# Kernel tuning notes

Hardware: AMD Instinct MI355X
Metric: run time of the kernel (lower is better)

## Reference

```python
import jax, jax.numpy as jnp
import numpy as np

N_NODES = 50000


def gcn_conv(x, W, b, src, dst, n_nodes):
    """PyG GCNConv: h = D^-1/2 (A + I) D^-1/2 (x W) + b, with self-loops."""
    h = x @ W  # [N, out]
    loop = jnp.arange(n_nodes, dtype=src.dtype)
    s = jnp.concatenate([src, loop])  # [E+N]
    d = jnp.concatenate([dst, loop])
    # degree of destination nodes (self-loops guarantee deg >= 1)
    deg = jax.ops.segment_sum(jnp.ones_like(d, dtype=h.dtype), d, num_segments=n_nodes)
    dinv = jax.lax.rsqrt(deg)  # deg >= 1 so safe
    norm = dinv[s] * dinv[d]  # [E+N]
    msg = h[s] * norm[:, None]  # gather + scale (per-edge messages)
    out = jax.ops.segment_sum(msg, d, num_segments=n_nodes)  # scatter-add
    return out + b


def setup_inputs() -> dict:
    key = jax.random.key(0)
    ks = jax.random.split(key, 8)
    in_d, hid, out_d = 128, 128, 64
    x = jax.random.normal(ks[0], (N_NODES, in_d), dtype=jnp.float32)
    edge_index = jax.random.randint(ks[1], (2, 800000), 0, N_NODES, dtype=jnp.int64)
    def glorot(k, fan_in, fan_out):
        lim = float(np.sqrt(6.0 / (fan_in + fan_out)))
        return jax.random.uniform(k, (fan_in, fan_out), jnp.float32, -lim, lim)
    return {
        "x": x,
        "edge_index": edge_index,
        "W1": glorot(ks[2], in_d, hid),
        "b1": jnp.zeros((hid,), jnp.float32),
        "W2": glorot(ks[3], hid, hid),
        "b2": jnp.zeros((hid,), jnp.float32),
        "W3": glorot(ks[4], hid, out_d),
        "b3": jnp.zeros((out_d,), jnp.float32),
    }


def reference(x, edge_index, W1, b1, W2, b2, W3, b3):
    src, dst = edge_index[0], edge_index[1]
    n = x.shape[0]
    h = jax.nn.relu(gcn_conv(x, W1, b1, src, dst, n))
    h = jax.nn.relu(gcn_conv(h, W2, b2, src, dst, n))
    return gcn_conv(h, W3, b3, src, dst, n)
```

## Files before the change

kernel.cpp:

```cpp
#include <hip/hip_runtime.h>
#include <stdint.h>
#include <stddef.h>

#define EE 800000
#define CAP 64
#define FB_G 256

typedef __attribute__((ext_vector_type(8))) short bf16x8;
typedef __attribute__((ext_vector_type(4))) float f32x4;

__device__ __forceinline__ float bflo(uint32_t p) { return __uint_as_float(p << 16); }
__device__ __forceinline__ float bfhi(uint32_t p) { return __uint_as_float(p & 0xffff0000u); }
__device__ __forceinline__ unsigned short f2bf(float v) {
  uint32_t b = __float_as_uint(v);
  b += 0x7fffu + ((b >> 16) & 1u);
  return (unsigned short)(b >> 16);
}

__device__ __forceinline__ void wt_work(int idx, const float* W1, const float* W2,
                                        const float* W3, unsigned short* Wt1,
                                        unsigned short* Wt2, unsigned short* Wt3) {
  if (idx < 16384) {
    int k = idx >> 7, n = idx & 127;
    Wt1[n * 128 + k] = f2bf(W1[idx]);
  } else if (idx < 32768) {
    int l = idx - 16384, k = l >> 7, n = l & 127;
    Wt2[n * 128 + k] = f2bf(W2[l]);
  } else if (idx < 40960) {
    int l = idx - 32768, k = l >> 6, n = l & 63;
    Wt3[n * 128 + k] = f2bf(W3[l]);
  }
}

__global__ void k15_fillslot(const int* ei, int* cnt, int* slots, int E, int N,
                             int* viol, const float* W1, const float* W2,
                             const float* W3, unsigned short* Wt1,
                             unsigned short* Wt2, unsigned short* Wt3) {
  if ((int)blockIdx.x >= 8 * FB_G) {
    wt_work(((int)blockIdx.x - 8 * FB_G) * 256 + threadIdx.x, W1, W2, W3, Wt1,
            Wt2, Wt3);
    return;
  }
  const int p = (int)blockIdx.x & 7;
  const int cb = (int)blockIdx.x >> 3;
  const int lo = (int)(((long long)N * p) >> 3);
  const int hi = (int)(((long long)N * (p + 1)) >> 3);
  const bool is64 =
      ((ei[1] | ei[3] | ei[5] | ei[7] | ei[9] | ei[11] | ei[13] | ei[15]) == 0);
  const uint2* e64 = (const uint2*)ei;
  const int step = FB_G * 256;

  int e = cb * 256 + (int)threadIdx.x;
  if (e >= E) return;
  int d = is64 ? (int)e64[(size_t)E + e].x : ei[(size_t)E + e];
  for (;;) {
    int e2 = e + step;
    int d2 = 0;
    if (e2 < E) d2 = is64 ? (int)e64[(size_t)E + e2].x : ei[(size_t)E + e2];
    if (p == 0 && (unsigned)d >= (unsigned)N) atomicOr(viol, 1);
    if (d >= lo && d < hi) {
      int s = is64 ? (int)e64[(size_t)e].x : ei[e];
      if ((unsigned)s >= (unsigned)N) {
        atomicOr(viol, 1);
      } else {
        int pos = atomicAdd(&cnt[d], 1);
        if (pos < CAP) slots[(size_t)d * CAP + pos] = s;
      }
    }
    if (e2 >= E) break;
    e = e2;
    d = d2;
  }
}

__global__ __launch_bounds__(256) void k12_wt(const float* W1, const float* W2,
                                              const float* W3, unsigned short* Wt1,
                                              unsigned short* Wt2, unsigned short* Wt3) {
  wt_work(blockIdx.x * 256 + threadIdx.x, W1, W2, W3, Wt1, Wt2, Wt3);
}

__global__ void k12_hist(const int* ei, int* cnt, int E, int N, int* viol) {
  bool is64 = ((ei[1] | ei[3] | ei[5] | ei[7] | ei[9] | ei[11] | ei[13] | ei[15]) == 0);
  if (blockIdx.x == 0 && threadIdx.x == 0) viol[1] = is64 ? 1 : 0;
  int e = blockIdx.x * 256 + threadIdx.x;
  if (e >= E) return;
  int s, d;
  if (is64) {
    const uint2* e64 = (const uint2*)ei;
    s = (int)e64[e].x;
    d = (int)e64[(size_t)E + e].x;
  } else {
    s = ei[e];
    d = ei[(size_t)E + e];
  }
  if ((unsigned)s >= (unsigned)N || (unsigned)d >= (unsigned)N) {
    atomicOr(viol, 1);
    return;
  }
  atomicAdd(&cnt[d], 1);
}

__global__ __launch_bounds__(256) void k12_scanA(const int* cnt, int* partial, int N) {
  __shared__ int sc[256];
  int t = threadIdx.x;
  int n = blockIdx.x * 256 + t;
  sc[t] = (n < N) ? cnt[n] : 0;
  __syncthreads();
  for (int s = 128; s > 0; s >>= 1) {
    if (t < s) sc[t] += sc[t + s];
    __syncthreads();
  }
  if (t == 0) partial[blockIdx.x] = sc[0];
}

__global__ __launch_bounds__(256) void k12_scanB(int* partial, int* off, int nsb,
                                                 int N, int E, int* viol) {
  __shared__ int sc[256];
  int t = threadIdx.x;
  int v = (t < nsb) ? partial[t] : 0;
  sc[t] = v;
  __syncthreads();
  for (int d = 1; d < 256; d <<= 1) {
    int w = (t >= d) ? sc[t - d] : 0;
    __syncthreads();
    sc[t] += w;
    __syncthreads();
  }
  if (t < nsb) partial[t] = sc[t] - v;
  if (t == 255) {
    off[N] = sc[255];
    if (sc[255] != E) atomicOr(viol, 4);
  }
}

__global__ __launch_bounds__(256) void k12_scanC(const int* cnt, const int* partial,
                                                 int* off, int* cur, float* dinv, int N) {
  __shared__ int sc[256];
  int t = threadIdx.x;
  int n = blockIdx.x * 256 + t;
  int v = (n < N) ? cnt[n] : 0;
  sc[t] = v;
  __syncthreads();
  for (int d = 1; d < 256; d <<= 1) {
    int w = (t >= d) ? sc[t - d] : 0;
    __syncthreads();
    sc[t] += w;
    __syncthreads();
  }
  if (n < N) {
    int o = partial[blockIdx.x] + sc[t] - v;
    off[n] = o;
    cur[n] = o;
    dinv[n] = rsqrtf((float)(v + 1));
  }
}

__global__ void k12_fillcsr(const int* ei, int* cur, int* adj, int E, int N,
                            const int* viol) {
  int is64 = viol[1];
  int e = blockIdx.x * 256 + threadIdx.x;
  if (e >= E) return;
  int s, d;
  if (is64) {
    const uint2* e64 = (const uint2*)ei;
    s = (int)e64[e].x;
    d = (int)e64[(size_t)E + e].x;
  } else {
    s = ei[e];
    d = ei[(size_t)E + e];
  }
  if ((unsigned)s >= (unsigned)N || (unsigned)d >= (unsigned)N) return;
  int pos = atomicAdd(&cur[d], 1);
  adj[pos] = s;
}

__global__ __launch_bounds__(256) void k12_gemmX(const float* __restrict__ X,
                                                 const unsigned short* __restrict__ Wt,
                                                 unsigned short* __restrict__ OUT,
                                                 int M) {
  const int tid = threadIdx.x;
  const int wid = tid >> 6, lane = tid & 63;
  const int quad = lane >> 4, r16 = lane & 15;
  const int m0 = blockIdx.x * 64 + wid * 16;
  const int mrow = m0 + r16;

  f32x4 acc[8];
#pragma unroll
  for (int ct = 0; ct < 8; ++ct) acc[ct] = {0.f, 0.f, 0.f, 0.f};

#pragma unroll
  for (int kk = 0; kk < 4; ++kk) {
    bf16x8 a = {0, 0, 0, 0, 0, 0, 0, 0};
    if (mrow < M) {
      const float* xp = X + (size_t)mrow * 128 + kk * 32 + quad * 8;
      float4 u0 = *(const float4*)xp;
      float4 u1 = *(const float4*)(xp + 4);
      a[0] = (short)f2bf(u0.x); a[1] = (short)f2bf(u0.y);
      a[2] = (short)f2bf(u0.z); a[3] = (short)f2bf(u0.w);
      a[4] = (short)f2bf(u1.x); a[5] = (short)f2bf(u1.y);
      a[6] = (short)f2bf(u1.z); a[7] = (short)f2bf(u1.w);
    }
#pragma unroll
    for (int ct = 0; ct < 8; ++ct) {
      bf16x8 b = *(const bf16x8*)(Wt + (size_t)(ct * 16 + r16) * 128 + kk * 32 + quad * 8);
      acc[ct] = __builtin_amdgcn_mfma_f32_16x16x32_bf16(a, b, acc[ct], 0, 0, 0);
    }
  }
#pragma unroll
  for (int ct = 0; ct < 8; ++ct) {
    int col = ct * 16 + r16;
#pragma unroll
    for (int r = 0; r < 4; ++r) {
      int row = m0 + quad * 4 + r;
      if (row < M) OUT[(size_t)row * 128 + col] = f2bf(acc[ct][r]);
    }
  }
}

template <int F>
__global__ __launch_bounds__(256) void k12_gemmB(const unsigned short* __restrict__ X,
                                                 const unsigned short* __restrict__ Wt,
                                                 unsigned short* __restrict__ OUT,
                                                 int M) {
  const int tid = threadIdx.x;
  const int wid = tid >> 6, lane = tid & 63;
  const int quad = lane >> 4, r16 = lane & 15;
  const int m0 = blockIdx.x * 64 + wid * 16;
  const int mrow = m0 + r16;
  constexpr int CT = F / 16;

  f32x4 acc[CT];
#pragma unroll
  for (int ct = 0; ct < CT; ++ct) acc[ct] = {0.f, 0.f, 0.f, 0.f};

#pragma unroll
  for (int kk = 0; kk < 4; ++kk) {
    bf16x8 a = {0, 0, 0, 0, 0, 0, 0, 0};
    if (mrow < M) a = *(const bf16x8*)(X + (size_t)mrow * 128 + kk * 32 + quad * 8);
#pragma unroll
    for (int ct = 0; ct < CT; ++ct) {
      bf16x8 b = *(const bf16x8*)(Wt + (size_t)(ct * 16 + r16) * 128 + kk * 32 + quad * 8);
      acc[ct] = __builtin_amdgcn_mfma_f32_16x16x32_bf16(a, b, acc[ct], 0, 0, 0);
    }
  }
#pragma unroll
  for (int ct = 0; ct < CT; ++ct) {
    int col = ct * 16 + r16;
#pragma unroll
    for (int r = 0; r < 4; ++r) {
      int row = m0 + quad * 4 + r;
      if (row < M) OUT[(size_t)row * F + col] = f2bf(acc[ct][r]);
    }
  }
}

template <int SLOT>
__global__ __launch_bounds__(256) void k15_agg128(
    const unsigned short* __restrict__ t, const int* __restrict__ cntoff,
    const int* __restrict__ adj, const float* __restrict__ dinv,
    const float* __restrict__ bias, unsigned short* __restrict__ out,
    int N, int* __restrict__ viol) {
  __shared__ uint2 sm[4][68];
  const int wid = (int)threadIdx.x >> 6;
  const int lane = (int)threadIdx.x & 63;
  const int g = lane >> 4, l16 = lane & 15;
  const int i = blockIdx.x * 4 + wid;
  if (i >= N) return;

  int j0, deg;
  float di;
  if (SLOT) {
    int c = cntoff[i];
    di = rsqrtf((float)(c + 1));
    if (c > CAP) {
      if (lane == 0) atomicOr(viol, 2);
      c = CAP;
    }
    deg = c;
    j0 = i * CAP;
  } else {
    j0 = cntoff[i];
    deg = cntoff[i + 1] - j0;
    di = dinv[i];
  }

  const int L = deg + 1;
  const uint4* rows = (const uint4*)t;
  float a0 = 0.f, a1 = 0.f, a2 = 0.f, a3 = 0.f;
  float a4 = 0.f, a5 = 0.f, a6 = 0.f, a7 = 0.f;

  for (int jb = 0; jb < L; jb += 64) {
    int v = jb + lane;
    uint2 ent;
    ent.x = 0u;
    ent.y = 0u;
    if (v == 0) {
      ent.x = (uint32_t)i;
      ent.y = __float_as_uint(di);
    } else if (v <= deg) {
      int s = adj[j0 + v - 1];
      float w = SLOT ? rsqrtf((float)(cntoff[s] + 1)) : dinv[s];
      ent.x = (uint32_t)s;
      ent.y = __float_as_uint(w);
    }
    sm[wid][lane] = ent;
    int nb2 = L - jb;
    if (nb2 > 64) nb2 = 64;
    int r4 = (nb2 + 3) >> 2;
    int b = 0;
    for (; b + 2 <= r4; b += 2) {
      uint2 s0 = sm[wid][b * 4 + g];
      uint2 s1 = sm[wid][b * 4 + 4 + g];
      uint4 p0 = rows[(size_t)s0.x * 16 + l16];
      uint4 p1 = rows[(size_t)s1.x * 16 + l16];
      float w0 = __uint_as_float(s0.y), w1 = __uint_as_float(s1.y);
      a0 = fmaf(w0, bflo(p0.x), a0); a1 = fmaf(w0, bfhi(p0.x), a1);
      a2 = fmaf(w0, bflo(p0.y), a2); a3 = fmaf(w0, bfhi(p0.y), a3);
      a4 = fmaf(w0, bflo(p0.z), a4); a5 = fmaf(w0, bfhi(p0.z), a5);
      a6 = fmaf(w0, bflo(p0.w), a6); a7 = fmaf(w0, bfhi(p0.w), a7);
      a0 = fmaf(w1, bflo(p1.x), a0); a1 = fmaf(w1, bfhi(p1.x), a1);
      a2 = fmaf(w1, bflo(p1.y), a2); a3 = fmaf(w1, bfhi(p1.y), a3);
      a4 = fmaf(w1, bflo(p1.z), a4); a5 = fmaf(w1, bfhi(p1.z), a5);
      a6 = fmaf(w1, bflo(p1.w), a6); a7 = fmaf(w1, bfhi(p1.w), a7);
    }
    if (b < r4) {
      uint2 s0 = sm[wid][b * 4 + g];
      uint4 p0 = rows[(size_t)s0.x * 16 + l16];
      float w0 = __uint_as_float(s0.y);
      a0 = fmaf(w0, bflo(p0.x), a0); a1 = fmaf(w0, bfhi(p0.x), a1);
      a2 = fmaf(w0, bflo(p0.y), a2); a3 = fmaf(w0, bfhi(p0.y), a3);
      a4 = fmaf(w0, bflo(p0.z), a4); a5 = fmaf(w0, bfhi(p0.z), a5);
      a6 = fmaf(w0, bflo(p0.w), a6); a7 = fmaf(w0, bfhi(p0.w), a7);
    }
  }
#pragma unroll
  for (int sx = 16; sx < 64; sx <<= 1) {
    a0 += __shfl_xor(a0, sx); a1 += __shfl_xor(a1, sx);
    a2 += __shfl_xor(a2, sx); a3 += __shfl_xor(a3, sx);
    a4 += __shfl_xor(a4, sx); a5 += __shfl_xor(a5, sx);
    a6 += __shfl_xor(a6, sx); a7 += __shfl_xor(a7, sx);
  }
  if (g == 0) {
    const float4* bf = (const float4*)bias;
    float4 b0 = bf[l16 * 2], b1 = bf[l16 * 2 + 1];
    a0 = fmaxf(fmaf(a0, di, b0.x), 0.f);
    a1 = fmaxf(fmaf(a1, di, b0.y), 0.f);
    a2 = fmaxf(fmaf(a2, di, b0.z), 0.f);
    a3 = fmaxf(fmaf(a3, di, b0.w), 0.f);
    a4 = fmaxf(fmaf(a4, di, b1.x), 0.f);
    a5 = fmaxf(fmaf(a5, di, b1.y), 0.f);
    a6 = fmaxf(fmaf(a6, di, b1.z), 0.f);
    a7 = fmaxf(fmaf(a7, di, b1.w), 0.f);
    uint4 pk;
    pk.x = (uint32_t)f2bf(a0) | ((uint32_t)f2bf(a1) << 16);
    pk.y = (uint32_t)f2bf(a2) | ((uint32_t)f2bf(a3) << 16);
    pk.z = (uint32_t)f2bf(a4) | ((uint32_t)f2bf(a5) << 16);
    pk.w = (uint32_t)f2bf(a6) | ((uint32_t)f2bf(a7) << 16);
    ((uint4*)out)[(size_t)i * 16 + l16] = pk;
  }
}

template <int SLOT>
__global__ __launch_bounds__(256) void k15_agg64(
    const unsigned short* __restrict__ t, const int* __restrict__ cntoff,
    const int* __restrict__ adj, const float* __restrict__ dinv,
    const float* __restrict__ bias, float* __restrict__ out,
    int N, int* __restrict__ viol) {
  __shared__ uint2 sm[4][68];
  const int wid = (int)threadIdx.x >> 6;
  const int lane = (int)threadIdx.x & 63;
  const int g = lane >> 4, l16 = lane & 15;
  const int i = blockIdx.x * 4 + wid;
  if (i >= N) return;

  int j0, deg;
  float di;
  if (SLOT) {
    int c = cntoff[i];
    di = rsqrtf((float)(c + 1));
    if (c > CAP) {
      if (lane == 0) atomicOr(viol, 2);
      c = CAP;
    }
    deg = c;
    j0 = i * CAP;
  } else {
    j0 = cntoff[i];
    deg = cntoff[i + 1] - j0;
    di = dinv[i];
  }

  const int L = deg + 1;
  const uint2* rows = (const uint2*)t;
  float a0 = 0.f, a1 = 0.f, a2 = 0.f, a3 = 0.f;

  for (int jb = 0; jb < L; jb += 64) {
    int v = jb + lane;
    uint2 ent;
    ent.x = 0u;
    ent.y = 0u;
    if (v == 0) {
      ent.x = (uint32_t)i;
      ent.y = __float_as_uint(di);
    } else if (v <= deg) {
      int s = adj[j0 + v - 1];
      float w = SLOT ? rsqrtf((float)(cntoff[s] + 1)) : dinv[s];
      ent.x = (uint32_t)s;
      ent.y = __float_as_uint(w);
    }
    sm[wid][lane] = ent;
    int nb2 = L - jb;
    if (nb2 > 64) nb2 = 64;
    int r4 = (nb2 + 3) >> 2;
    int b = 0;
    for (; b + 2 <= r4; b += 2) {
      uint2 s0 = sm[wid][b * 4 + g];
      uint2 s1 = sm[wid][b * 4 + 4 + g];
      uint2 p0 = rows[(size_t)s0.x * 16 + l16];
      uint2 p1 = rows[(size_t)s1.x * 16 + l16];
      float w0 = __uint_as_float(s0.y), w1 = __uint_as_float(s1.y);
      a0 = fmaf(w0, bflo(p0.x), a0); a1 = fmaf(w0, bfhi(p0.x), a1);
      a2 = fmaf(w0, bflo(p0.y), a2); a3 = fmaf(w0, bfhi(p0.y), a3);
      a0 = fmaf(w1, bflo(p1.x), a0); a1 = fmaf(w1, bfhi(p1.x), a1);
      a2 = fmaf(w1, bflo(p1.y), a2); a3 = fmaf(w1, bfhi(p1.y), a3);
    }
    if (b < r4) {
      uint2 s0 = sm[wid][b * 4 + g];
      uint2 p0 = rows[(size_t)s0.x * 16 + l16];
      float w0 = __uint_as_float(s0.y);
      a0 = fmaf(w0, bflo(p0.x), a0); a1 = fmaf(w0, bfhi(p0.x), a1);
      a2 = fmaf(w0, bflo(p0.y), a2); a3 = fmaf(w0, bfhi(p0.y), a3);
    }
  }
#pragma unroll
  for (int sx = 16; sx < 64; sx <<= 1) {
    a0 += __shfl_xor(a0, sx); a1 += __shfl_xor(a1, sx);
    a2 += __shfl_xor(a2, sx); a3 += __shfl_xor(a3, sx);
  }
  if (g == 0) {
    float4 b0 = ((const float4*)bias)[l16];
    float4 r;
    r.x = fmaf(a0, di, b0.x);
    r.y = fmaf(a1, di, b0.y);
    r.z = fmaf(a2, di, b0.z);
    r.w = fmaf(a3, di, b0.w);
    ((float4*)out)[(size_t)i * 16 + l16] = r;
  }
}

__global__ void k12_sent(const int* viol, float* out, int hc4, int hc7) {
  if (threadIdx.x != 0 || blockIdx.x != 0) return;
  int v = viol[0];
  if (v & 1) out[1] = 1200.f;
  if (v & 2) out[6] = 2200.f;
  if (v & 4) out[2] = 1300.f;
  if (hc4)   out[4] = 1800.f;
  if (hc7)   out[7] = 2400.f;
}

__global__ void k12_wsrep(float* out, float code) {
  if (threadIdx.x == 0 && blockIdx.x == 0) out[3] = code;
}

extern "C" void kernel_launch(void* const* d_in, const int* in_sizes, int n_in,
                              void* d_out, int out_size, void* d_ws, size_t ws_size,
                              hipStream_t stream) {
  if (n_in < 8) {
    hipMemsetAsync(d_out, 0, (size_t)out_size * 4, stream);
    k12_wsrep<<<1, 64, 0, stream>>>((float*)d_out, 2500.f + n_in);
    return;
  }
  const float* x  = (const float*)d_in[0];
  const int* ei   = (const int*)d_in[1];
  const float* W1 = (const float*)d_in[2];
  const float* b1 = (const float*)d_in[3];
  const float* W2 = (const float*)d_in[4];
  const float* b2 = (const float*)d_in[5];
  const float* W3 = (const float*)d_in[6];
  const float* b3 = (const float*)d_in[7];

  const int N = in_sizes[0] / 128;
  int hc7 = (N == 50000) ? 0 : 1;
  int E = in_sizes[1] / 2;
  int hc4 = 0;
  if (in_sizes[1] == 2 * EE || in_sizes[1] == 4 * EE) E = EE;
  else hc4 = 1;

  char* base = (char*)d_ws;
  size_t o = 0;
  auto carve = [&](size_t bytes) {
    char* q = base + o;
    o += (bytes + 255) & ~(size_t)255;
    return q;
  };
  int* viol   = (int*)carve(256);
  int* cnt    = (int*)carve((size_t)N * 4);
  float* dinv = (float*)carve((size_t)N * 4);
  unsigned short* Wt1 = (unsigned short*)carve(16384 * 2);
  unsigned short* Wt2 = (unsigned short*)carve(16384 * 2);
  unsigned short* Wt3 = (unsigned short*)carve(8192 * 2);
  unsigned short* T   = (unsigned short*)carve((size_t)N * 128 * 2);
  unsigned short* B   = (unsigned short*)carve((size_t)N * 128 * 2);
  size_t common = o;

  int* slots = (int*)carve((size_t)N * CAP * 4);
  size_t slot_need = o;
  o = common;
  int* off     = (int*)carve((size_t)(N + 1) * 4);
  int* cur     = (int*)carve((size_t)N * 4);
  int* partial = (int*)carve(256 * 4);
  int* adj     = (int*)carve((size_t)E * 4);
  size_t csr_need = o;

  bool use_slot = (ws_size >= slot_need);
  if (!use_slot && ws_size < csr_need) {
    hipMemsetAsync(d_out, 0, (size_t)out_size * 4, stream);
    int wsmb = (int)(ws_size >> 20);
    if (wsmb > 20000) wsmb = 20000;
    k12_wsrep<<<1, 64, 0, stream>>>((float*)d_out, 4000.f + (float)wsmb);
    return;
  }

  hipMemsetAsync(cnt, 0, (size_t)N * 4, stream);
  hipMemsetAsync(viol, 0, 16, stream);

  const int ablocks = (N + 3) / 4;
  const int gblocks = (N + 63) / 64;
  const int nfb = (E + 255) / 256;

  if (use_slot) {
    k15_fillslot<<<8 * FB_G + 160, 256, 0, stream>>>(ei, cnt, slots, E, N, viol,
                                                     W1, W2, W3, Wt1, Wt2, Wt3);

    k12_gemmX<<<gblocks, 256, 0, stream>>>(x, Wt1, T, N);
    k15_agg128<1><<<ablocks, 256, 0, stream>>>(T, cnt, slots, nullptr, b1, B, N, viol);
    k12_gemmB<128><<<gblocks, 256, 0, stream>>>(B, Wt2, T, N);
    k15_agg128<1><<<ablocks, 256, 0, stream>>>(T, cnt, slots, nullptr, b2, B, N, viol);
    k12_gemmB<64><<<gblocks, 256, 0, stream>>>(B, Wt3, T, N);
    k15_agg64<1><<<ablocks, 256, 0, stream>>>(T, cnt, slots, nullptr, b3,
                                              (float*)d_out, N, viol);
  } else {
    const int nsb = (N + 255) / 256;
    k12_wt<<<160, 256, 0, stream>>>(W1, W2, W3, Wt1, Wt2, Wt3);
    k12_hist<<<nfb, 256, 0, stream>>>(ei, cnt, E, N, viol);
    k12_scanA<<<nsb, 256, 0, stream>>>(cnt, partial, N);
    k12_scanB<<<1, 256, 0, stream>>>(partial, off, nsb, N, E, viol);
    k12_scanC<<<nsb, 256, 0, stream>>>(cnt, partial, off, cur, dinv, N);
    k12_fillcsr<<<nfb, 256, 0, stream>>>(ei, cur, adj, E, N, viol);

    k12_gemmX<<<gblocks, 256, 0, stream>>>(x, Wt1, T, N);
    k15_agg128<0><<<ablocks, 256, 0, stream>>>(T, off, adj, dinv, b1, B, N, viol);
    k12_gemmB<128><<<gblocks, 256, 0, stream>>>(B, Wt2, T, N);
    k15_agg128<0><<<ablocks, 256, 0, stream>>>(T, off, adj, dinv, b2, B, N, viol);
    k12_gemmB<64><<<gblocks, 256, 0, stream>>>(B, Wt3, T, N);
    k15_agg64<0><<<ablocks, 256, 0, stream>>>(T, off, adj, dinv, b3,
                                              (float*)d_out, N, viol);
  }
  k12_sent<<<1, 64, 0, stream>>>(viol, (float*)d_out, hc4, hc7);
}
```

Before: 270.5 us.

## Fuse whole GCN pipeline into one persistent cooperative megakernel with grid syncs

Replaces the sequence of memsets and seven kernel launches on the slot path with a single cooperative persistent kernel that runs zeroing, weight transpose, slot fill, three GEMMs and three aggregations, separated by grid-wide syncs. Each stage loops over its tiles or nodes with a grid-stride pattern. This removes per-launch overhead and inter-kernel gaps. In exchange, occupancy is capped by the persistent grid and each phase pays a grid barrier. Tail imbalance within a phase can no longer overlap with the next phase.

```diff
diff --git a/kernel.cpp b/kernel.cpp
--- a/kernel.cpp
+++ b/kernel.cpp
@@ -1,6 +1,9 @@
 #include <hip/hip_runtime.h>
+#include <hip/hip_cooperative_groups.h>
 #include <stdint.h>
 #include <stddef.h>
+
+namespace cg = cooperative_groups;
 
 #define EE 800000
 #define CAP 64
@@ -32,156 +35,14 @@
   }
 }
 
-__global__ void k15_fillslot(const int* ei, int* cnt, int* slots, int E, int N,
-                             int* viol, const float* W1, const float* W2,
-                             const float* W3, unsigned short* Wt1,
-                             unsigned short* Wt2, unsigned short* Wt3) {
-  if ((int)blockIdx.x >= 8 * FB_G) {
-    wt_work(((int)blockIdx.x - 8 * FB_G) * 256 + threadIdx.x, W1, W2, W3, Wt1,
-            Wt2, Wt3);
-    return;
-  }
-  const int p = (int)blockIdx.x & 7;
-  const int cb = (int)blockIdx.x >> 3;
-  const int lo = (int)(((long long)N * p) >> 3);
-  const int hi = (int)(((long long)N * (p + 1)) >> 3);
-  const bool is64 =
-      ((ei[1] | ei[3] | ei[5] | ei[7] | ei[9] | ei[11] | ei[13] | ei[15]) == 0);
-  const uint2* e64 = (const uint2*)ei;
-  const int step = FB_G * 256;
-
-  int e = cb * 256 + (int)threadIdx.x;
-  if (e >= E) return;
-  int d = is64 ? (int)e64[(size_t)E + e].x : ei[(size_t)E + e];
-  for (;;) {
-    int e2 = e + step;
-    int d2 = 0;
-    if (e2 < E) d2 = is64 ? (int)e64[(size_t)E + e2].x : ei[(size_t)E + e2];
-    if (p == 0 && (unsigned)d >= (unsigned)N) atomicOr(viol, 1);
-    if (d >= lo && d < hi) {
-      int s = is64 ? (int)e64[(size_t)e].x : ei[e];
-      if ((unsigned)s >= (unsigned)N) {
-        atomicOr(viol, 1);
-      } else {
-        int pos = atomicAdd(&cnt[d], 1);
-        if (pos < CAP) slots[(size_t)d * CAP + pos] = s;
-      }
-    }
-    if (e2 >= E) break;
-    e = e2;
-    d = d2;
-  }
-}
-
-__global__ __launch_bounds__(256) void k12_wt(const float* W1, const float* W2,
-                                              const float* W3, unsigned short* Wt1,
-                                              unsigned short* Wt2, unsigned short* Wt3) {
-  wt_work(blockIdx.x * 256 + threadIdx.x, W1, W2, W3, Wt1, Wt2, Wt3);
-}
-
-__global__ void k12_hist(const int* ei, int* cnt, int E, int N, int* viol) {
-  bool is64 = ((ei[1] | ei[3] | ei[5] | ei[7] | ei[9] | ei[11] | ei[13] | ei[15]) == 0);
-  if (blockIdx.x == 0 && threadIdx.x == 0) viol[1] = is64 ? 1 : 0;
-  int e = blockIdx.x * 256 + threadIdx.x;
-  if (e >= E) return;
-  int s, d;
-  if (is64) {
-    const uint2* e64 = (const uint2*)ei;
-    s = (int)e64[e].x;
-    d = (int)e64[(size_t)E + e].x;
-  } else {
-    s = ei[e];
-    d = ei[(size_t)E + e];
-  }
-  if ((unsigned)s >= (unsigned)N || (unsigned)d >= (unsigned)N) {
-    atomicOr(viol, 1);
-    return;
-  }
-  atomicAdd(&cnt[d], 1);
-}
-
-__global__ __launch_bounds__(256) void k12_scanA(const int* cnt, int* partial, int N) {
-  __shared__ int sc[256];
-  int t = threadIdx.x;
-  int n = blockIdx.x * 256 + t;
-  sc[t] = (n < N) ? cnt[n] : 0;
-  __syncthreads();
-  for (int s = 128; s > 0; s >>= 1) {
-    if (t < s) sc[t] += sc[t + s];
-    __syncthreads();
-  }
-  if (t == 0) partial[blockIdx.x] = sc[0];
-}
-
-__global__ __launch_bounds__(256) void k12_scanB(int* partial, int* off, int nsb,
-                                                 int N, int E, int* viol) {
-  __shared__ int sc[256];
-  int t = threadIdx.x;
-  int v = (t < nsb) ? partial[t] : 0;
-  sc[t] = v;
-  __syncthreads();
-  for (int d = 1; d < 256; d <<= 1) {
-    int w = (t >= d) ? sc[t - d] : 0;
-    __syncthreads();
-    sc[t] += w;
-    __syncthreads();
-  }
-  if (t < nsb) partial[t] = sc[t] - v;
-  if (t == 255) {
-    off[N] = sc[255];
-    if (sc[255] != E) atomicOr(viol, 4);
-  }
-}
-
-__global__ __launch_bounds__(256) void k12_scanC(const int* cnt, const int* partial,
-                                                 int* off, int* cur, float* dinv, int N) {
-  __shared__ int sc[256];
-  int t = threadIdx.x;
-  int n = blockIdx.x * 256 + t;
-  int v = (n < N) ? cnt[n] : 0;
-  sc[t] = v;
-  __syncthreads();
-  for (int d = 1; d < 256; d <<= 1) {
-    int w = (t >= d) ? sc[t - d] : 0;
-    __syncthreads();
-    sc[t] += w;
-    __syncthreads();
-  }
-  if (n < N) {
-    int o = partial[blockIdx.x] + sc[t] - v;
-    off[n] = o;
-    cur[n] = o;
-    dinv[n] = rsqrtf((float)(v + 1));
-  }
-}
-
-__global__ void k12_fillcsr(const int* ei, int* cur, int* adj, int E, int N,
-                            const int* viol) {
-  int is64 = viol[1];
-  int e = blockIdx.x * 256 + threadIdx.x;
-  if (e >= E) return;
-  int s, d;
-  if (is64) {
-    const uint2* e64 = (const uint2*)ei;
-    s = (int)e64[e].x;
-    d = (int)e64[(size_t)E + e].x;
-  } else {
-    s = ei[e];
-    d = ei[(size_t)E + e];
-  }
-  if ((unsigned)s >= (unsigned)N || (unsigned)d >= (unsigned)N) return;
-  int pos = atomicAdd(&cur[d], 1);
-  adj[pos] = s;
-}
-
-__global__ __launch_bounds__(256) void k12_gemmX(const float* __restrict__ X,
-                                                 const unsigned short* __restrict__ Wt,
-                                                 unsigned short* __restrict__ OUT,
-                                                 int M) {
-  const int tid = threadIdx.x;
+
+__device__ __forceinline__ void dev_gemmX(int tile, int tid,
+                                          const float* __restrict__ X,
+                                          const unsigned short* __restrict__ Wt,
+                                          unsigned short* __restrict__ OUT, int M) {
   const int wid = tid >> 6, lane = tid & 63;
   const int quad = lane >> 4, r16 = lane & 15;
-  const int m0 = blockIdx.x * 64 + wid * 16;
+  const int m0 = tile * 64 + wid * 16;
   const int mrow = m0 + r16;
 
   f32x4 acc[8];
@@ -218,14 +79,13 @@
 }
 
 template <int F>
-__global__ __launch_bounds__(256) void k12_gemmB(const unsigned short* __restrict__ X,
-                                                 const unsigned short* __restrict__ Wt,
-                                                 unsigned short* __restrict__ OUT,
-                                                 int M) {
-  const int tid = threadIdx.x;
+__device__ __forceinline__ void dev_gemmB(int tile, int tid,
+                                          const unsigned short* __restrict__ X,
+                                          const unsigned short* __restrict__ Wt,
+                                          unsigned short* __restrict__ OUT, int M) {
   const int wid = tid >> 6, lane = tid & 63;
   const int quad = lane >> 4, r16 = lane & 15;
-  const int m0 = blockIdx.x * 64 + wid * 16;
+  const int m0 = tile * 64 + wid * 16;
   const int mrow = m0 + r16;
   constexpr int CT = F / 16;
 
@@ -255,17 +115,14 @@
 }
 
 template <int SLOT>
-__global__ __launch_bounds__(256) void k15_agg128(
-    const unsigned short* __restrict__ t, const int* __restrict__ cntoff,
-    const int* __restrict__ adj, const float* __restrict__ dinv,
-    const float* __restrict__ bias, unsigned short* __restrict__ out,
-    int N, int* __restrict__ viol) {
-  __shared__ uint2 sm[4][68];
-  const int wid = (int)threadIdx.x >> 6;
-  const int lane = (int)threadIdx.x & 63;
+__device__ __forceinline__ void dev_agg128(
+    int i, int tid, uint2 (*sm)[68], const unsigned short* __restrict__ t,
+    const int* __restrict__ cntoff, const int* __restrict__ adj,
+    const float* __restrict__ dinv, const float* __restrict__ bias,
+    unsigned short* __restrict__ out, int N, int* __restrict__ viol) {
+  const int wid = tid >> 6;
+  const int lane = tid & 63;
   const int g = lane >> 4, l16 = lane & 15;
-  const int i = blockIdx.x * 4 + wid;
-  if (i >= N) return;
 
   int j0, deg;
   float di;
@@ -361,17 +218,14 @@
 }
 
 template <int SLOT>
-__global__ __launch_bounds__(256) void k15_agg64(
-    const unsigned short* __restrict__ t, const int* __restrict__ cntoff,
-    const int* __restrict__ adj, const float* __restrict__ dinv,
-    const float* __restrict__ bias, float* __restrict__ out,
-    int N, int* __restrict__ viol) {
-  __shared__ uint2 sm[4][68];
-  const int wid = (int)threadIdx.x >> 6;
-  const int lane = (int)threadIdx.x & 63;
+__device__ __forceinline__ void dev_agg64(
+    int i, int tid, uint2 (*sm)[68], const unsigned short* __restrict__ t,
+    const int* __restrict__ cntoff, const int* __restrict__ adj,
+    const float* __restrict__ dinv, const float* __restrict__ bias,
+    float* __restrict__ out, int N, int* __restrict__ viol) {
+  const int wid = tid >> 6;
+  const int lane = tid & 63;
   const int g = lane >> 4, l16 = lane & 15;
-  const int i = blockIdx.x * 4 + wid;
-  if (i >= N) return;
 
   int j0, deg;
   float di;
@@ -446,6 +300,290 @@
     r.w = fmaf(a3, di, b0.w);
     ((float4*)out)[(size_t)i * 16 + l16] = r;
   }
+}
+
+struct KArgs {
+  const float* x;
+  const int* ei;
+  const float* W1; const float* b1;
+  const float* W2; const float* b2;
+  const float* W3; const float* b3;
+  int* cnt; int* slots;
+  unsigned short* Wt1; unsigned short* Wt2; unsigned short* Wt3;
+  unsigned short* T; unsigned short* B;
+  float* out; int* viol;
+  int E; int N; int hc4; int hc7;
+};
+
+__global__ __launch_bounds__(256, 4) void k16_mega(KArgs a) {
+  cg::grid_group gg = cg::this_grid();
+  __shared__ uint2 sm[4][68];
+  const int tid = (int)threadIdx.x;
+  const int bid = (int)blockIdx.x;
+  const int NB = (int)gridDim.x;
+  const int gtid = bid * 256 + tid;
+  const int gsz = NB * 256;
+
+  for (int i = gtid; i < a.N; i += gsz) a.cnt[i] = 0;
+  if (gtid < 8) a.viol[gtid] = 0;
+  for (int idx = gtid; idx < 40960; idx += gsz)
+    wt_work(idx, a.W1, a.W2, a.W3, a.Wt1, a.Wt2, a.Wt3);
+  gg.sync();
+
+  {
+    const int p = bid & 7;
+    const int lo = (int)(((long long)a.N * p) >> 3);
+    const int hi = (int)(((long long)a.N * (p + 1)) >> 3);
+    const bool is64 = ((a.ei[1] | a.ei[3] | a.ei[5] | a.ei[7] | a.ei[9] |
+                        a.ei[11] | a.ei[13] | a.ei[15]) == 0);
+    const uint2* e64 = (const uint2*)a.ei;
+    const int step = (NB >> 3) * 256;
+    for (int e = (bid >> 3) * 256 + tid; e < a.E; e += step) {
+      int d = is64 ? (int)e64[(size_t)a.E + e].x : a.ei[(size_t)a.E + e];
+      if (p == 0 && (unsigned)d >= (unsigned)a.N) atomicOr(a.viol, 1);
+      if (d < lo || d >= hi) continue;
+      int s = is64 ? (int)e64[e].x : a.ei[e];
+      if ((unsigned)s >= (unsigned)a.N) {
+        atomicOr(a.viol, 1);
+        continue;
+      }
+      int pos = atomicAdd(&a.cnt[d], 1);
+      if (pos < CAP) a.slots[(size_t)d * CAP + pos] = s;
+    }
+  }
+  gg.sync();
+
+  {
+    const int tiles = (a.N + 63) >> 6;
+    for (int t0 = bid; t0 < tiles; t0 += NB) dev_gemmX(t0, tid, a.x, a.Wt1, a.T, a.N);
+  }
+  gg.sync();
+
+  {
+    const int quads = (a.N + 3) >> 2;
+    const int wid = tid >> 6;
+    for (int q = bid; q < quads; q += NB) {
+      int i = q * 4 + wid;
+      if (i < a.N)
+        dev_agg128<1>(i, tid, sm, a.T, a.cnt, a.slots, nullptr, a.b1, a.B, a.N, a.viol);
+    }
+  }
+  gg.sync();
+
+  {
+    const int tiles = (a.N + 63) >> 6;
+    for (int t0 = bid; t0 < tiles; t0 += NB) dev_gemmB<128>(t0, tid, a.B, a.Wt2, a.T, a.N);
+  }
+  gg.sync();
+
+  {
+    const int quads = (a.N + 3) >> 2;
+    const int wid = tid >> 6;
+    for (int q = bid; q < quads; q += NB) {
+      int i = q * 4 + wid;
+      if (i < a.N)
+        dev_agg128<1>(i, tid, sm, a.T, a.cnt, a.slots, nullptr, a.b2, a.B, a.N, a.viol);
+    }
+  }
+  gg.sync();
+
+  {
+    const int tiles = (a.N + 63) >> 6;
+    for (int t0 = bid; t0 < tiles; t0 += NB) dev_gemmB<64>(t0, tid, a.B, a.Wt3, a.T, a.N);
+  }
+  gg.sync();
+
+  {
+    const int quads = (a.N + 3) >> 2;
+    const int wid = tid >> 6;
+    for (int q = bid; q < quads; q += NB) {
+      int i = q * 4 + wid;
+      if (i < a.N)
+        dev_agg64<1>(i, tid, sm, a.T, a.cnt, a.slots, nullptr, a.b3, a.out, a.N, a.viol);
+    }
+  }
+  gg.sync();
+
+  if (bid == 0 && tid == 0) {
+    int v = atomicOr(a.viol, 0);
+    if (v & 1) a.out[1] = 1200.f;
+    if (v & 2) a.out[6] = 2200.f;
+    if (v & 4) a.out[2] = 1300.f;
+    if (a.hc4) a.out[4] = 1800.f;
+    if (a.hc7) a.out[7] = 2400.f;
+  }
+}
+
+__global__ void k15_fillslot(const int* ei, int* cnt, int* slots, int E, int N,
+                             int* viol, const float* W1, const float* W2,
+                             const float* W3, unsigned short* Wt1,
+                             unsigned short* Wt2, unsigned short* Wt3) {
+  if ((int)blockIdx.x >= 8 * FB_G) {
+    wt_work(((int)blockIdx.x - 8 * FB_G) * 256 + threadIdx.x, W1, W2, W3, Wt1,
+            Wt2, Wt3);
+    return;
+  }
+  const int p = (int)blockIdx.x & 7;
+  const int cb = (int)blockIdx.x >> 3;
+  const int lo = (int)(((long long)N * p) >> 3);
+  const int hi = (int)(((long long)N * (p + 1)) >> 3);
+  const bool is64 =
+      ((ei[1] | ei[3] | ei[5] | ei[7] | ei[9] | ei[11] | ei[13] | ei[15]) == 0);
+  const uint2* e64 = (const uint2*)ei;
+  const int step = FB_G * 256;
+
+  for (int e = cb * 256 + (int)threadIdx.x; e < E; e += step) {
+    int d = is64 ? (int)e64[(size_t)E + e].x : ei[(size_t)E + e];
+    if (p == 0 && (unsigned)d >= (unsigned)N) atomicOr(viol, 1);
+    if (d < lo || d >= hi) continue;
+    int s = is64 ? (int)e64[e].x : ei[e];
+    if ((unsigned)s >= (unsigned)N) {
+      atomicOr(viol, 1);
+      continue;
+    }
+    int pos = atomicAdd(&cnt[d], 1);
+    if (pos < CAP) slots[(size_t)d * CAP + pos] = s;
+  }
+}
+
+__global__ __launch_bounds__(256) void k12_wt(const float* W1, const float* W2,
+                                              const float* W3, unsigned short* Wt1,
+                                              unsigned short* Wt2, unsigned short* Wt3) {
+  wt_work(blockIdx.x * 256 + threadIdx.x, W1, W2, W3, Wt1, Wt2, Wt3);
+}
+
+__global__ void k12_hist(const int* ei, int* cnt, int E, int N, int* viol) {
+  bool is64 = ((ei[1] | ei[3] | ei[5] | ei[7] | ei[9] | ei[11] | ei[13] | ei[15]) == 0);
+  if (blockIdx.x == 0 && threadIdx.x == 0) viol[1] = is64 ? 1 : 0;
+  int e = blockIdx.x * 256 + threadIdx.x;
+  if (e >= E) return;
+  int s, d;
+  if (is64) {
+    const uint2* e64 = (const uint2*)ei;
+    s = (int)e64[e].x;
+    d = (int)e64[(size_t)E + e].x;
+  } else {
+    s = ei[e];
+    d = ei[(size_t)E + e];
+  }
+  if ((unsigned)s >= (unsigned)N || (unsigned)d >= (unsigned)N) {
+    atomicOr(viol, 1);
+    return;
+  }
+  atomicAdd(&cnt[d], 1);
+}
+
+__global__ __launch_bounds__(256) void k12_scanA(const int* cnt, int* partial, int N) {
+  __shared__ int sc[256];
+  int t = threadIdx.x;
+  int n = blockIdx.x * 256 + t;
+  sc[t] = (n < N) ? cnt[n] : 0;
+  __syncthreads();
+  for (int s = 128; s > 0; s >>= 1) {
+    if (t < s) sc[t] += sc[t + s];
+    __syncthreads();
+  }
+  if (t == 0) partial[blockIdx.x] = sc[0];
+}
+
+__global__ __launch_bounds__(256) void k12_scanB(int* partial, int* off, int nsb,
+                                                 int N, int E, int* viol) {
+  __shared__ int sc[256];
+  int t = threadIdx.x;
+  int v = (t < nsb) ? partial[t] : 0;
+  sc[t] = v;
+  __syncthreads();
+  for (int d = 1; d < 256; d <<= 1) {
+    int w = (t >= d) ? sc[t - d] : 0;
+    __syncthreads();
+    sc[t] += w;
+    __syncthreads();
+  }
+  if (t < nsb) partial[t] = sc[t] - v;
+  if (t == 255) {
+    off[N] = sc[255];
+    if (sc[255] != E) atomicOr(viol, 4);
+  }
+}
+
+__global__ __launch_bounds__(256) void k12_scanC(const int* cnt, const int* partial,
+                                                 int* off, int* cur, float* dinv, int N) {
+  __shared__ int sc[256];
+  int t = threadIdx.x;
+  int n = blockIdx.x * 256 + t;
+  int v = (n < N) ? cnt[n] : 0;
+  sc[t] = v;
+  __syncthreads();
+  for (int d = 1; d < 256; d <<= 1) {
+    int w = (t >= d) ? sc[t - d] : 0;
+    __syncthreads();
+    sc[t] += w;
+    __syncthreads();
+  }
+  if (n < N) {
+    int o = partial[blockIdx.x] + sc[t] - v;
+    off[n] = o;
+    cur[n] = o;
+    dinv[n] = rsqrtf((float)(v + 1));
+  }
+}
+
+__global__ void k12_fillcsr(const int* ei, int* cur, int* adj, int E, int N,
+                            const int* viol) {
+  int is64 = viol[1];
+  int e = blockIdx.x * 256 + threadIdx.x;
+  if (e >= E) return;
+  int s, d;
+  if (is64) {
+    const uint2* e64 = (const uint2*)ei;
+    s = (int)e64[e].x;
+    d = (int)e64[(size_t)E + e].x;
+  } else {
+    s = ei[e];
+    d = ei[(size_t)E + e];
+  }
+  if ((unsigned)s >= (unsigned)N || (unsigned)d >= (unsigned)N) return;
+  int pos = atomicAdd(&cur[d], 1);
+  adj[pos] = s;
+}
+
+__global__ __launch_bounds__(256) void k12_gemmX(const float* __restrict__ X,
+                                                 const unsigned short* __restrict__ Wt,
+                                                 unsigned short* __restrict__ OUT,
+                                                 int M) {
+  dev_gemmX(blockIdx.x, threadIdx.x, X, Wt, OUT, M);
+}
+
+template <int F>
+__global__ __launch_bounds__(256) void k12_gemmB(const unsigned short* __restrict__ X,
+                                                 const unsigned short* __restrict__ Wt,
+                                                 unsigned short* __restrict__ OUT,
+                                                 int M) {
+  dev_gemmB<F>(blockIdx.x, threadIdx.x, X, Wt, OUT, M);
+}
+
+template <int SLOT>
+__global__ __launch_bounds__(256) void k15_agg128(
+    const unsigned short* __restrict__ t, const int* __restrict__ cntoff,
+    const int* __restrict__ adj, const float* __restrict__ dinv,
+    const float* __restrict__ bias, unsigned short* __restrict__ out,
+    int N, int* __restrict__ viol) {
+  __shared__ uint2 sm[4][68];
+  int i = blockIdx.x * 4 + ((int)threadIdx.x >> 6);
+  if (i < N)
+    dev_agg128<SLOT>(i, threadIdx.x, sm, t, cntoff, adj, dinv, bias, out, N, viol);
+}
+
+template <int SLOT>
+__global__ __launch_bounds__(256) void k15_agg64(
+    const unsigned short* __restrict__ t, const int* __restrict__ cntoff,
+    const int* __restrict__ adj, const float* __restrict__ dinv,
+    const float* __restrict__ bias, float* __restrict__ out,
+    int N, int* __restrict__ viol) {
+  __shared__ uint2 sm[4][68];
+  int i = blockIdx.x * 4 + ((int)threadIdx.x >> 6);
+  if (i < N)
+    dev_agg64<SLOT>(i, threadIdx.x, sm, t, cntoff, adj, dinv, bias, out, N, viol);
 }
 
 __global__ void k12_sent(const int* viol, float* out, int hc4, int hc7) {
@@ -521,25 +659,48 @@
     return;
   }
 
-  hipMemsetAsync(cnt, 0, (size_t)N * 4, stream);
-  hipMemsetAsync(viol, 0, 16, stream);
-
   const int ablocks = (N + 3) / 4;
   const int gblocks = (N + 63) / 64;
   const int nfb = (E + 255) / 256;
 
   if (use_slot) {
-    k15_fillslot<<<8 * FB_G + 160, 256, 0, stream>>>(ei, cnt, slots, E, N, viol,
-                                                     W1, W2, W3, Wt1, Wt2, Wt3);
-
-    k12_gemmX<<<gblocks, 256, 0, stream>>>(x, Wt1, T, N);
-    k15_agg128<1><<<ablocks, 256, 0, stream>>>(T, cnt, slots, nullptr, b1, B, N, viol);
-    k12_gemmB<128><<<gblocks, 256, 0, stream>>>(B, Wt2, T, N);
-    k15_agg128<1><<<ablocks, 256, 0, stream>>>(T, cnt, slots, nullptr, b2, B, N, viol);
-    k12_gemmB<64><<<gblocks, 256, 0, stream>>>(B, Wt3, T, N);
-    k15_agg64<1><<<ablocks, 256, 0, stream>>>(T, cnt, slots, nullptr, b3,
-                                              (float*)d_out, N, viol);
+    int dev = 0;
+    hipGetDevice(&dev);
+    int maxb = 0, ncu = 0;
+    hipError_t q1 = hipOccupancyMaxActiveBlocksPerMultiprocessor(&maxb, k16_mega, 256, 0);
+    hipError_t q2 = hipDeviceGetAttribute(&ncu, hipDeviceAttributeMultiprocessorCount, dev);
+    int grid = 0;
+    if (q1 == hipSuccess && q2 == hipSuccess) {
+      grid = maxb * ncu;
+      if (grid > 2048) grid = 2048;
+      grid &= ~7;
+    }
+    bool launched = false;
+    if (grid >= 8) {
+      KArgs ka = {x, ei, W1, b1, W2, b2, W3, b3, cnt, slots,
+                  Wt1, Wt2, Wt3, T, B, (float*)d_out, viol, E, N, hc4, hc7};
+      void* args[] = {&ka};
+      hipError_t le = hipLaunchCooperativeKernel((const void*)k16_mega, dim3(grid),
+                                                 dim3(256), args, 0, stream);
+      launched = (le == hipSuccess);
+    }
+    if (!launched) {
+      hipMemsetAsync(cnt, 0, (size_t)N * 4, stream);
+      hipMemsetAsync(viol, 0, 16, stream);
+      k15_fillslot<<<8 * FB_G + 160, 256, 0, stream>>>(ei, cnt, slots, E, N, viol,
+                                                       W1, W2, W3, Wt1, Wt2, Wt3);
+      k12_gemmX<<<gblocks, 256, 0, stream>>>(x, Wt1, T, N);
+      k15_agg128<1><<<ablocks, 256, 0, stream>>>(T, cnt, slots, nullptr, b1, B, N, viol);
+      k12_gemmB<128><<<gblocks, 256, 0, stream>>>(B, Wt2, T, N);
+      k15_agg128<1><<<ablocks, 256, 0, stream>>>(T, cnt, slots, nullptr, b2, B, N, viol);
+      k12_gemmB<64><<<gblocks, 256, 0, stream>>>(B, Wt3, T, N);
+      k15_agg64<1><<<ablocks, 256, 0, stream>>>(T, cnt, slots, nullptr, b3,
+                                                (float*)d_out, N, viol);
+      k12_sent<<<1, 64, 0, stream>>>(viol, (float*)d_out, hc4, hc7);
+    }
   } else {
+    hipMemsetAsync(cnt, 0, (size_t)N * 4, stream);
+    hipMemsetAsync(viol, 0, 16, stream);
     const int nsb = (N + 255) / 256;
     k12_wt<<<160, 256, 0, stream>>>(W1, W2, W3, Wt1, Wt2, Wt3);
     k12_hist<<<nfb, 256, 0, stream>>>(ei, cnt, E, N, viol);
@@ -555,6 +716,6 @@
     k12_gemmB<64><<<gblocks, 256, 0, stream>>>(B, Wt3, T, N);
     k15_agg64<0><<<ablocks, 256, 0, stream>>>(T, off, adj, dinv, b3,
                                               (float*)d_out, N, viol);
-  }
-  k12_sent<<<1, 64, 0, stream>>>(viol, (float*)d_out, hc4, hc7);
-}
+    k12_sent<<<1, 64, 0, stream>>>(viol, (float*)d_out, hc4, hc7);
+  }
+}
```

Result: slower. 883.6 us (+226.7%).
